# Kernel optimization log

Measured on AMD Instinct MI355X. Metric: run time of the kernel, lower is better.

## Reference

```python
import jax, jax.numpy as jnp
import numpy as np

SHAPES = ((100, 100), (50, 50), (25, 25))  # (H, W) per level
B, D, NH, HD, NL, NP, DFF = 4, 256, 8, 32, 3, 4, 1024
L = sum(h * w for h, w in SHAPES)  # 13125
EPS = 1e-5


def _layer_norm(x, g, b):
    m = jnp.mean(x, axis=-1, keepdims=True)
    v = jnp.var(x, axis=-1, keepdims=True)
    return (x - m) * jax.lax.rsqrt(v + EPS) * g + b


def _grid_sample_bilinear(img, grid):
    """img: [N,C,H,W]; grid: [N,Lq,P,2] in [-1,1]; align_corners=False, zero pad.
    Returns [N,C,Lq,P]."""
    N, C, H, W = img.shape
    x = ((grid[..., 0] + 1.0) * W - 1.0) * 0.5
    y = ((grid[..., 1] + 1.0) * H - 1.0) * 0.5
    x0 = jnp.floor(x); y0 = jnp.floor(y)
    x1 = x0 + 1.0; y1 = y0 + 1.0
    wx1 = x - x0; wx0 = 1.0 - wx1
    wy1 = y - y0; wy0 = 1.0 - wy1
    flat = img.reshape(N, C, H * W)

    def gather(ix, iy):
        valid = ((ix >= 0) & (ix < W) & (iy >= 0) & (iy < H)).astype(img.dtype)
        ii = (jnp.clip(iy, 0, H - 1).astype(jnp.int32) * W
              + jnp.clip(ix, 0, W - 1).astype(jnp.int32))  # [N,Lq,P]
        idx = jnp.broadcast_to(ii.reshape(N, 1, -1), (N, C, ii.shape[1] * ii.shape[2]))
        vals = jnp.take_along_axis(flat, idx, axis=2).reshape(N, C, ii.shape[1], ii.shape[2])
        return vals * valid[:, None]

    out = (gather(x0, y0) * (wx0 * wy0)[:, None]
           + gather(x1, y0) * (wx1 * wy0)[:, None]
           + gather(x0, y1) * (wx0 * wy1)[:, None]
           + gather(x1, y1) * (wx1 * wy1)[:, None])
    return out


def _ms_deform_attn_core(value, loc, attn):
    """value: [B,L,NH,HD]; loc: [B,Lq,NH,NL,NP,2] in [0,1]; attn: [B,Lq,NH,NL,NP]."""
    Bn, Lq = loc.shape[0], loc.shape[1]
    grids = 2.0 * loc - 1.0
    start = 0
    samples = []
    for lid, (H, W) in enumerate(SHAPES):
        v = value[:, start:start + H * W]            # [B,HW,NH,HD]
        start += H * W
        v = v.transpose(0, 2, 3, 1).reshape(Bn * NH, HD, H, W)
        g = grids[:, :, :, lid].transpose(0, 2, 1, 3, 4).reshape(Bn * NH, Lq, NP, 2)
        samples.append(_grid_sample_bilinear(v, g))  # [B*NH,HD,Lq,NP]
    sv = jnp.stack(samples, axis=-2).reshape(Bn * NH, HD, Lq, NL * NP)
    a = attn.transpose(0, 2, 1, 3, 4).reshape(Bn * NH, 1, Lq, NL * NP)
    out = (sv * a).sum(-1)                            # [B*NH,HD,Lq]
    return out.reshape(Bn, NH * HD, Lq).transpose(0, 2, 1)


def setup_inputs() -> dict:
    key = jax.random.key(0)
    ks = jax.random.split(key, 16)
    f32 = jnp.float32
    inp = {
        'src': jax.random.normal(ks[0], (B, L, D), f32),
        'pos': jax.random.normal(ks[1], (B, L, D), f32),
        'reference_points': jax.random.uniform(ks[2], (B, L, NL, 2), f32),
        'Wv': jax.random.normal(ks[3], (D, D), f32) * 0.02,
        'bv': jnp.zeros((D,), f32),
        'Woff': jax.random.normal(ks[4], (D, NH * NL * NP * 2), f32) * 0.02,
        'boff': jax.random.normal(ks[5], (NH * NL * NP * 2,), f32) * 0.5,
        'Wattn': jax.random.normal(ks[6], (D, NH * NL * NP), f32) * 0.02,
        'battn': jnp.zeros((NH * NL * NP,), f32),
        'Wout': jax.random.normal(ks[7], (D, D), f32) * 0.02,
        'bout': jnp.zeros((D,), f32),
        'g1': jnp.ones((D,), f32), 'b1': jnp.zeros((D,), f32),
        'Wff1': jax.random.normal(ks[8], (D, DFF), f32) * 0.02,
        'bff1': jnp.zeros((DFF,), f32),
        'Wff2': jax.random.normal(ks[9], (DFF, D), f32) * 0.02,
        'bff2': jnp.zeros((D,), f32),
        'g2': jnp.ones((D,), f32), 'b2': jnp.zeros((D,), f32),
    }
    return inp


def reference(src, pos, reference_points, Wv, bv, Woff, boff, Wattn, battn,
              Wout, bout, g1, b1, Wff1, bff1, Wff2, bff2, g2, b2):
    # DeformableTransformerEncoderLayer forward (eval mode: dropout = identity)
    q = src + pos
    value = (src @ Wv + bv).reshape(B, L, NH, HD)
    off = (q @ Woff + boff).reshape(B, L, NH, NL, NP, 2)
    attn = jax.nn.softmax((q @ Wattn + battn).reshape(B, L, NH, NL * NP), axis=-1)
    attn = attn.reshape(B, L, NH, NL, NP)
    norm = jnp.array([[w, h] for h, w in SHAPES], dtype=src.dtype)  # [NL,2] = (W,H)
    loc = reference_points[:, :, None, :, None, :] + off / norm[None, None, None, :, None, :]
    attn_out = _ms_deform_attn_core(value, loc, attn) @ Wout + bout
    x = _layer_norm(src + attn_out, g1, b1)
    ff = jax.nn.relu(x @ Wff1 + bff1) @ Wff2 + bff2
    return _layer_norm(x + ff, g2, b2)
```

## Files before the change

### kernel.cpp

```cpp
#include <hip/hip_runtime.h>


#define BLTOK 52500
#define MP    52608
#define LSP   13125

using short8  = __attribute__((ext_vector_type(8))) short;
using ushort8v= __attribute__((ext_vector_type(8))) unsigned short;
using f32x4   = __attribute__((ext_vector_type(4))) float;
using fl2     = __attribute__((ext_vector_type(2))) float;

__device__ __forceinline__ ushort f2b(float f) {
  union { float f; unsigned u; } x; x.f = f;
  unsigned r = (x.u + 0x7fffu + ((x.u >> 16) & 1u)) >> 16;
  return (ushort)r;
}
__device__ __forceinline__ float b2f(ushort h) {
  union { unsigned u; float f; } x; x.u = ((unsigned)h) << 16;
  return x.f;
}

#define GLDS16(gp, lp) __builtin_amdgcn_global_load_lds( \
    (const __attribute__((address_space(1))) void*)(gp), \
    (__attribute__((address_space(3))) void*)(lp), 16, 0, 0)

__global__ __launch_bounds__(256) void prep_weights(
    const float* __restrict__ Wv, const float* __restrict__ Woff,
    const float* __restrict__ Wattn, const float* __restrict__ Wout,
    const float* __restrict__ Wff1, const float* __restrict__ Wff2,
    const float* __restrict__ boff, const float* __restrict__ battn,
    ushort* __restrict__ wv_t, ushort* __restrict__ wcat_t,
    ushort* __restrict__ wout_t, ushort* __restrict__ wff1_t,
    ushort* __restrict__ wff2_t, float* __restrict__ bcat)
{
  int i = blockIdx.x * 256 + threadIdx.x;
  if (i < 65536) {
    int n = i >> 8, k = i & 255;
    wv_t[i] = f2b(Wv[k * 256 + n]);
    return;
  }
  int j = i - 65536;
  if (j < 98304) {
    int n = j >> 8, k = j & 255;
    float v = (n < 192) ? Woff[k * 192 + n]
            : (n < 288) ? Wattn[k * 96 + (n - 192)] : 0.f;
    wcat_t[j] = f2b(v);
    return;
  }
  j -= 98304;
  if (j < 65536) {
    int n = j >> 8, k = j & 255;
    wout_t[j] = f2b(Wout[k * 256 + n]);
    return;
  }
  j -= 65536;
  if (j < 262144) {
    int n = j >> 8, k = j & 255;
    wff1_t[j] = f2b(Wff1[k * 1024 + n]);
    return;
  }
  j -= 262144;
  if (j < 262144) {
    int n = j >> 10, k = j & 1023;
    wff2_t[j] = f2b(Wff2[k * 256 + n]);
    return;
  }
  j -= 262144;
  if (j < 384) bcat[j] = (j < 192) ? boff[j] : (j < 288) ? battn[j - 192] : 0.f;
}

__global__ __launch_bounds__(256) void prep_act(
    const float* __restrict__ src, const float* __restrict__ pos,
    ushort* __restrict__ src_bf, ushort* __restrict__ q_bf)
{
  const size_t e = ((size_t)blockIdx.x * 256 + threadIdx.x) * 4;
  if (e >= (size_t)MP * 256) return;
  ushort4 sb, qb;
  if (e < (size_t)BLTOK * 256) {
    const float4 s = *(const float4*)(src + e);
    const float4 p = *(const float4*)(pos + e);
    sb.x = f2b(s.x); sb.y = f2b(s.y); sb.z = f2b(s.z); sb.w = f2b(s.w);
    qb.x = f2b(s.x + p.x); qb.y = f2b(s.y + p.y);
    qb.z = f2b(s.z + p.z); qb.w = f2b(s.w + p.w);
  } else {
    sb.x = sb.y = sb.z = sb.w = 0;
    qb.x = qb.y = qb.z = qb.w = 0;
  }
  *(ushort4*)(src_bf + e) = sb;
  *(ushort4*)(q_bf + e) = qb;
}

template <int EPI>
__global__ __launch_bounds__(256) void gemm128(
    const ushort* __restrict__ A, const ushort* __restrict__ Bt,
    const float* __restrict__ bias, const float* __restrict__ addf,
    const ushort* __restrict__ addb, ushort* __restrict__ C,
    int Mact, int Nact, int Nstr, int K)
{
  __shared__ __align__(16) ushort sm[16384];
  ushort* As = sm;
  ushort* Bs = sm + 8192;
  float*  epf = (float*)sm;
  const int tid = threadIdx.x;
  const int wave = tid >> 6, lane = tid & 63;
  const int n0 = blockIdx.x * 128, m0 = blockIdx.y * 128;
  const int srow = lane >> 2, skc = (lane & 3) * 8;
  const ushort* Ag = A + (size_t)(m0 + wave * 32 + srow) * K + skc;
  const ushort* Bg = Bt + (size_t)(n0 + wave * 32 + srow) * K + skc;
  const int quad = lane >> 4, l16 = lane & 15;
  const int wm = (wave & 1) * 64, wn = (wave >> 1) * 64;
  f32x4 acc[4][4] = {};

#define STAGE(buf, kk) { \
    ushort* la = As + (buf) * 4096 + wave * 1024; \
    ushort* lb = Bs + (buf) * 4096 + wave * 1024; \
    GLDS16(Ag + (kk), la); \
    GLDS16(Ag + (kk) + 16 * K, la + 512); \
    GLDS16(Bg + (kk), lb); \
    GLDS16(Bg + (kk) + 16 * K, lb + 512); }

  STAGE(0, 0);
  int cur = 0;
  for (int k0 = 0; k0 < K; k0 += 32) {
    __syncthreads();
    if (k0 + 32 < K) STAGE(cur ^ 1, k0 + 32);
    const ushort* Ab = As + cur * 4096;
    const ushort* Bb = Bs + cur * 4096;
    short8 af[4], bf[4];
#pragma unroll
    for (int i = 0; i < 4; i++)
      af[i] = *(const short8*)(&Ab[(wm + i * 16 + l16) * 32 + quad * 8]);
#pragma unroll
    for (int j = 0; j < 4; j++)
      bf[j] = *(const short8*)(&Bb[(wn + j * 16 + l16) * 32 + quad * 8]);
#pragma unroll
    for (int i = 0; i < 4; i++)
#pragma unroll
      for (int j = 0; j < 4; j++)
        acc[i][j] = __builtin_amdgcn_mfma_f32_16x16x32_bf16(af[i], bf[j],
                                                            acc[i][j], 0, 0, 0);
    cur ^= 1;
  }
#undef STAGE

  for (int half = 0; half < 2; half++) {
    __syncthreads();
    if ((wave & 1) == half) {
#pragma unroll
      for (int i = 0; i < 4; i++)
#pragma unroll
        for (int j = 0; j < 4; j++)
#pragma unroll
          for (int r = 0; r < 4; r++)
            epf[(i * 16 + quad * 4 + r) * 128 + wn + j * 16 + l16] = acc[i][j][r];
    }
    __syncthreads();
    const int gm0 = m0 + half * 64;
#pragma unroll
    for (int g = 0; g < 4; g++) {
      const int lrow = g * 16 + (tid >> 4);
      const int col0 = (tid & 15) * 8;
      const int grow = gm0 + lrow;
      const int gcol = n0 + col0;
      if (grow < Mact && gcol < Nact) {
        float v[8];
#pragma unroll
        for (int c = 0; c < 8; c++) v[c] = epf[lrow * 128 + col0 + c] + bias[gcol + c];
        const size_t idx = (size_t)grow * Nstr + gcol;
        if (EPI == 1) {
          const float4 a0 = *(const float4*)(addf + idx);
          const float4 a1 = *(const float4*)(addf + idx + 4);
          v[0] += a0.x; v[1] += a0.y; v[2] += a0.z; v[3] += a0.w;
          v[4] += a1.x; v[5] += a1.y; v[6] += a1.z; v[7] += a1.w;
        }
        if (EPI == 2) {
#pragma unroll
          for (int c = 0; c < 8; c++) v[c] = fmaxf(v[c], 0.f);
        }
        if (EPI == 3) {
          const ushort8v ab = *(const ushort8v*)(addb + idx);
#pragma unroll
          for (int c = 0; c < 8; c++) v[c] += b2f(ab[c]);
        }
        ushort8v o;
#pragma unroll
        for (int c = 0; c < 8; c++) o[c] = f2b(v[c]);
        *(ushort8v*)(C + idx) = o;
      }
    }
  }
}

__global__ __launch_bounds__(256) void deform_sample(
    const ushort* __restrict__ value, const ushort* __restrict__ oa_all,
    const float* __restrict__ refp, ushort* __restrict__ outb)
{
  const int tid = threadIdx.x;
  const int tok = blockIdx.x * 8 + (tid >> 5);
  if (tok >= BLTOK) return;
  const int b = tok / LSP;
  const int l = tid & 31;
  const int h = l >> 2;
  const ushort* oa = oa_all + (uint)tok * 320u;
  const float* rp = refp + (uint)tok * 6u;
  const uint base = (uint)b * (LSP * 256u) + (uint)(l * 8);
  const int Wl[3] = {100, 50, 25};
  const int Stl[3] = {0, 10000, 12500};

  const ushort* lg = oa + 192 + h * 12;
  float w[12], mx = -1e30f;
#pragma unroll
  for (int i = 0; i < 12; i++) { w[i] = b2f(lg[i]); mx = fmaxf(mx, w[i]); }
  float s = 0.f;
#pragma unroll
  for (int i = 0; i < 12; i++) { w[i] = expf(w[i] - mx); s += w[i]; }
  const float inv = 1.f / s;

  fl2 acc2[4] = {};
#pragma unroll
  for (int lid = 0; lid < 3; lid++) {
    const int W = Wl[lid], st = Stl[lid];
    const float Wf = (float)W;
    const float rx = rp[lid * 2], ry = rp[lid * 2 + 1];
#pragma unroll
    for (int p = 0; p < 4; p++) {
      const uint oxy = *(const uint*)(oa + h * 24 + lid * 8 + p * 2);
      union { uint u; float f; } ux, uy;
      ux.u = oxy << 16;
      uy.u = oxy & 0xffff0000u;
      const float aw = w[lid * 4 + p] * inv;
      const float x = (rx + ux.f / Wf) * Wf - 0.5f;
      const float y = (ry + uy.f / Wf) * Wf - 0.5f;
      const float x0f = floorf(x), y0f = floorf(y);
      const float wx1 = x - x0f, wy1 = y - y0f;
      const float wx0 = 1.f - wx1, wy0 = 1.f - wy1;
      const int ix0 = (int)x0f, iy0 = (int)y0f;
      const bool x0v = (ix0 >= 0) & (ix0 < W);
      const bool x1v = (ix0 + 1 >= 0) & (ix0 + 1 < W);
      const bool y0v = (iy0 >= 0) & (iy0 < W);
      const bool y1v = (iy0 + 1 >= 0) & (iy0 + 1 < W);
      const float ay0 = aw * wy0, ay1 = aw * wy1;
      const float w00 = (x0v & y0v) ? ay0 * wx0 : 0.f;
      const float w10 = (x1v & y0v) ? ay0 * wx1 : 0.f;
      const float w01 = (x0v & y1v) ? ay1 * wx0 : 0.f;
      const float w11 = (x1v & y1v) ? ay1 * wx1 : 0.f;
      const int ix0c = min(max(ix0, 0), W - 1);
      const int ix1c = min(max(ix0 + 1, 0), W - 1);
      const int iy0c = min(max(iy0, 0), W - 1);
      const int iy1c = min(max(iy0 + 1, 0), W - 1);
      const uint r00 = (uint)(st + iy0c * W + ix0c) * 256u;
      const uint r10 = (uint)(st + iy0c * W + ix1c) * 256u;
      const uint r01 = (uint)(st + iy1c * W + ix0c) * 256u;
      const uint r11 = (uint)(st + iy1c * W + ix1c) * 256u;
      const uint4 q00 = *(const uint4*)(value + base + r00);
      const uint4 q10 = *(const uint4*)(value + base + r10);
      const uint4 q01 = *(const uint4*)(value + base + r01);
      const uint4 q11 = *(const uint4*)(value + base + r11);
      const fl2 w00v = {w00, w00}, w10v = {w10, w10};
      const fl2 w01v = {w01, w01}, w11v = {w11, w11};
      const uint* u00 = (const uint*)&q00;
      const uint* u10 = (const uint*)&q10;
      const uint* u01 = (const uint*)&q01;
      const uint* u11 = (const uint*)&q11;
#pragma unroll
      for (int pp = 0; pp < 4; pp++) {
        union { uint u; float f; } a, bb2, cc, dd, a2, b2u, c2, d2;
        a.u  = u00[pp] << 16;  a2.u  = u00[pp] & 0xffff0000u;
        bb2.u= u10[pp] << 16;  b2u.u = u10[pp] & 0xffff0000u;
        cc.u = u01[pp] << 16;  c2.u  = u01[pp] & 0xffff0000u;
        dd.u = u11[pp] << 16;  d2.u  = u11[pp] & 0xffff0000u;
        fl2 v00 = {a.f, a2.f}, v10 = {bb2.f, b2u.f};
        fl2 v01 = {cc.f, c2.f}, v11 = {dd.f, d2.f};
        acc2[pp] += w00v * v00 + w10v * v10 + w01v * v01 + w11v * v11;
      }
    }
  }
  ushort4 o0, o1;
  o0.x = f2b(acc2[0].x); o0.y = f2b(acc2[0].y);
  o0.z = f2b(acc2[1].x); o0.w = f2b(acc2[1].y);
  o1.x = f2b(acc2[2].x); o1.y = f2b(acc2[2].y);
  o1.z = f2b(acc2[3].x); o1.w = f2b(acc2[3].y);
  ushort* op = outb + (uint)tok * 256u + (uint)(l * 8);
  *(ushort4*)op = o0;
  *(ushort4*)(op + 4) = o1;
}

template <int OUTF>
__global__ __launch_bounds__(256) void ln256(
    const ushort* __restrict__ in, const float* __restrict__ gg,
    const float* __restrict__ bb, ushort* __restrict__ outb,
    float* __restrict__ outf, int rows)
{
  const int wave = threadIdx.x >> 6, lane = threadIdx.x & 63;
  const int r = blockIdx.x * 4 + wave;
  if (r >= rows) return;
  const ushort* rowp = in + (size_t)r * 256;
  const ushort4 u = *(const ushort4*)(rowp + lane * 4);
  float v[4] = {b2f(u.x), b2f(u.y), b2f(u.z), b2f(u.w)};
  float s = v[0] + v[1] + v[2] + v[3];
  float s2 = v[0] * v[0] + v[1] * v[1] + v[2] * v[2] + v[3] * v[3];
#pragma unroll
  for (int o = 32; o > 0; o >>= 1) {
    s += __shfl_xor(s, o);
    s2 += __shfl_xor(s2, o);
  }
  const float mean = s * (1.f / 256.f);
  const float var = s2 * (1.f / 256.f) - mean * mean;
  const float rstd = rsqrtf(var + 1e-5f);
#pragma unroll
  for (int j = 0; j < 4; j++) {
    const int col = lane * 4 + j;
    const float o = (v[j] - mean) * rstd * gg[col] + bb[col];
    if (OUTF) outf[(size_t)r * 256 + col] = o;
    else outb[(size_t)r * 256 + col] = f2b(o);
  }
}

extern "C" void kernel_launch(void* const* d_in, const int* in_sizes, int n_in,
                              void* d_out, int out_size, void* d_ws, size_t ws_size,
                              hipStream_t stream)
{
  const float* src   = (const float*)d_in[0];
  const float* pos   = (const float*)d_in[1];
  const float* refp  = (const float*)d_in[2];
  const float* Wv    = (const float*)d_in[3];
  const float* bv    = (const float*)d_in[4];
  const float* Woff  = (const float*)d_in[5];
  const float* boff  = (const float*)d_in[6];
  const float* Wattn = (const float*)d_in[7];
  const float* battn = (const float*)d_in[8];
  const float* Wout  = (const float*)d_in[9];
  const float* bout  = (const float*)d_in[10];
  const float* g1    = (const float*)d_in[11];
  const float* b1    = (const float*)d_in[12];
  const float* Wff1  = (const float*)d_in[13];
  const float* bff1  = (const float*)d_in[14];
  const float* Wff2  = (const float*)d_in[15];
  const float* bff2  = (const float*)d_in[16];
  const float* g2    = (const float*)d_in[17];
  const float* b2    = (const float*)d_in[18];
  float* out = (float*)d_out;
  char* ws = (char*)d_ws;

  ushort* wcat_t = (ushort*)(ws + 0);
  ushort* wff1_t = (ushort*)(ws + 196608);
  ushort* wff2_t = (ushort*)(ws + 720896);
  float*  bcat   = (float*)(ws + 1245184);
  ushort* A1 = (ushort*)(ws + 1246720);
  ushort* A2 = (ushort*)(ws + 28182016);
  ushort* A3 = (ushort*)(ws + 55117312);
  ushort* A4 = (ushort*)(ws + 81997312);
  ushort* A5 = (ushort*)(ws + 115597312);
  ushort* wout_t = (ushort*)(ws + 223076352);
  ushort* wv_t   = (ushort*)(ws + 223207424);

  prep_weights<<<2946, 256, 0, stream>>>(Wv, Woff, Wattn, Wout, Wff1, Wff2,
                                         boff, battn,
                                         wv_t, wcat_t, wout_t, wff1_t, wff2_t, bcat);
  prep_act<<<MP / 4, 256, 0, stream>>>(src, pos, A1, A2);
  gemm128<0><<<dim3(2, MP / 128), 256, 0, stream>>>(A1, wv_t, bv, nullptr, nullptr,
                                                    A3, BLTOK, 256, 256, 256);
  gemm128<0><<<dim3(3, MP / 128), 256, 0, stream>>>(A2, wcat_t, bcat, nullptr, nullptr,
                                                    A4, BLTOK, 320, 320, 256);
  deform_sample<<<(BLTOK + 7) / 8, 256, 0, stream>>>(A3, A4, refp, A5);
  gemm128<3><<<dim3(2, MP / 128), 256, 0, stream>>>(A5, wout_t, bout, nullptr, A1,
                                                    A4, BLTOK, 256, 256, 256);
  ln256<0><<<BLTOK / 4, 256, 0, stream>>>(A4, g1, b1, A2, nullptr, BLTOK);
  gemm128<2><<<dim3(8, MP / 128), 256, 0, stream>>>(A2, wff1_t, bff1, nullptr, nullptr,
                                                    A5, MP, 1024, 1024, 256);
  gemm128<3><<<dim3(2, MP / 128), 256, 0, stream>>>(A5, wff2_t, bff2, nullptr, A2,
                                                    A3, BLTOK, 256, 256, 1024);
  ln256<1><<<BLTOK / 4, 256, 0, stream>>>(A3, g2, b2, nullptr, out, BLTOK);
}
```

Before: 478.5 us.

## Map one thread per head in deform sampling with vectorized offset loads

The deformable sampling kernel now gives each thread a whole head (32 channels) for one token, so one block covers 32 tokens instead of 8. Each thread computes the offsets and softmax for its head once, rather than four threads repeating that work. Offsets and logits come in with wide vector loads, and the location maths drops a divide and multiply because the normalisation cancels. The cost is four times as many gather loads and accumulators per thread, which raises register pressure and cuts memory-level parallelism across threads. It also uses fast exp and a hardware reciprocal.

```diff
diff --git a/kernel.cpp b/kernel.cpp
--- a/kernel.cpp
+++ b/kernel.cpp
@@ -17,6 +17,14 @@
 }
 __device__ __forceinline__ float b2f(ushort h) {
   union { unsigned u; float f; } x; x.u = ((unsigned)h) << 16;
+  return x.f;
+}
+__device__ __forceinline__ float blo(uint u) {
+  union { unsigned u; float f; } x; x.u = u << 16;
+  return x.f;
+}
+__device__ __forceinline__ float bhi(uint u) {
+  union { unsigned u; float f; } x; x.u = u & 0xffff0000u;
   return x.f;
 }
 
@@ -196,41 +204,51 @@
     const float* __restrict__ refp, ushort* __restrict__ outb)
 {
   const int tid = threadIdx.x;
-  const int tok = blockIdx.x * 8 + (tid >> 5);
+  const int tok = blockIdx.x * 32 + (tid >> 3);
   if (tok >= BLTOK) return;
   const int b = tok / LSP;
-  const int l = tid & 31;
-  const int h = l >> 2;
+  const int h = tid & 7;
   const ushort* oa = oa_all + (uint)tok * 320u;
   const float* rp = refp + (uint)tok * 6u;
-  const uint base = (uint)b * (LSP * 256u) + (uint)(l * 8);
+  const uint base = (uint)b * (LSP * 256u) + (uint)(h * 32);
+
+  const uint4 oq0 = *(const uint4*)(oa + h * 24);
+  const uint4 oq1 = *(const uint4*)(oa + h * 24 + 8);
+  const uint4 oq2 = *(const uint4*)(oa + h * 24 + 16);
+  const uint oxy[12] = {oq0.x, oq0.y, oq0.z, oq0.w,
+                        oq1.x, oq1.y, oq1.z, oq1.w,
+                        oq2.x, oq2.y, oq2.z, oq2.w};
+
+  const ushort* lgp = oa + 192 + h * 12;
+  const uint2 lq0 = *(const uint2*)(lgp);
+  const uint2 lq1 = *(const uint2*)(lgp + 4);
+  const uint2 lq2 = *(const uint2*)(lgp + 8);
+  float w[12] = {blo(lq0.x), bhi(lq0.x), blo(lq0.y), bhi(lq0.y),
+                 blo(lq1.x), bhi(lq1.x), blo(lq1.y), bhi(lq1.y),
+                 blo(lq2.x), bhi(lq2.x), blo(lq2.y), bhi(lq2.y)};
+  float mx = -1e30f;
+#pragma unroll
+  for (int i = 0; i < 12; i++) mx = fmaxf(mx, w[i]);
+  float s = 0.f;
+#pragma unroll
+  for (int i = 0; i < 12; i++) { w[i] = __expf(w[i] - mx); s += w[i]; }
+  const float inv = __builtin_amdgcn_rcpf(s);
+
   const int Wl[3] = {100, 50, 25};
   const int Stl[3] = {0, 10000, 12500};
-
-  const ushort* lg = oa + 192 + h * 12;
-  float w[12], mx = -1e30f;
-#pragma unroll
-  for (int i = 0; i < 12; i++) { w[i] = b2f(lg[i]); mx = fmaxf(mx, w[i]); }
-  float s = 0.f;
-#pragma unroll
-  for (int i = 0; i < 12; i++) { w[i] = expf(w[i] - mx); s += w[i]; }
-  const float inv = 1.f / s;
-
-  fl2 acc2[4] = {};
+  fl2 acc[16] = {};
 #pragma unroll
   for (int lid = 0; lid < 3; lid++) {
     const int W = Wl[lid], st = Stl[lid];
     const float Wf = (float)W;
-    const float rx = rp[lid * 2], ry = rp[lid * 2 + 1];
+    const float rxw = rp[lid * 2] * Wf - 0.5f;
+    const float ryw = rp[lid * 2 + 1] * Wf - 0.5f;
 #pragma unroll
     for (int p = 0; p < 4; p++) {
-      const uint oxy = *(const uint*)(oa + h * 24 + lid * 8 + p * 2);
-      union { uint u; float f; } ux, uy;
-      ux.u = oxy << 16;
-      uy.u = oxy & 0xffff0000u;
+      const uint o = oxy[lid * 4 + p];
       const float aw = w[lid * 4 + p] * inv;
-      const float x = (rx + ux.f / Wf) * Wf - 0.5f;
-      const float y = (ry + uy.f / Wf) * Wf - 0.5f;
+      const float x = rxw + blo(o);
+      const float y = ryw + bhi(o);
       const float x0f = floorf(x), y0f = floorf(y);
       const float wx1 = x - x0f, wy1 = y - y0f;
       const float wx0 = 1.f - wx1, wy0 = 1.f - wy1;
@@ -248,41 +266,44 @@
       const int ix1c = min(max(ix0 + 1, 0), W - 1);
       const int iy0c = min(max(iy0, 0), W - 1);
       const int iy1c = min(max(iy0 + 1, 0), W - 1);
-      const uint r00 = (uint)(st + iy0c * W + ix0c) * 256u;
-      const uint r10 = (uint)(st + iy0c * W + ix1c) * 256u;
-      const uint r01 = (uint)(st + iy1c * W + ix0c) * 256u;
-      const uint r11 = (uint)(st + iy1c * W + ix1c) * 256u;
-      const uint4 q00 = *(const uint4*)(value + base + r00);
-      const uint4 q10 = *(const uint4*)(value + base + r10);
-      const uint4 q01 = *(const uint4*)(value + base + r01);
-      const uint4 q11 = *(const uint4*)(value + base + r11);
+      const ushort* p00 = value + base + (uint)(st + iy0c * W + ix0c) * 256u;
+      const ushort* p10 = value + base + (uint)(st + iy0c * W + ix1c) * 256u;
+      const ushort* p01 = value + base + (uint)(st + iy1c * W + ix0c) * 256u;
+      const ushort* p11 = value + base + (uint)(st + iy1c * W + ix1c) * 256u;
       const fl2 w00v = {w00, w00}, w10v = {w10, w10};
       const fl2 w01v = {w01, w01}, w11v = {w11, w11};
-      const uint* u00 = (const uint*)&q00;
-      const uint* u10 = (const uint*)&q10;
-      const uint* u01 = (const uint*)&q01;
-      const uint* u11 = (const uint*)&q11;
-#pragma unroll
-      for (int pp = 0; pp < 4; pp++) {
-        union { uint u; float f; } a, bb2, cc, dd, a2, b2u, c2, d2;
-        a.u  = u00[pp] << 16;  a2.u  = u00[pp] & 0xffff0000u;
-        bb2.u= u10[pp] << 16;  b2u.u = u10[pp] & 0xffff0000u;
-        cc.u = u01[pp] << 16;  c2.u  = u01[pp] & 0xffff0000u;
-        dd.u = u11[pp] << 16;  d2.u  = u11[pp] & 0xffff0000u;
-        fl2 v00 = {a.f, a2.f}, v10 = {bb2.f, b2u.f};
-        fl2 v01 = {cc.f, c2.f}, v11 = {dd.f, d2.f};
-        acc2[pp] += w00v * v00 + w10v * v10 + w01v * v01 + w11v * v11;
+#pragma unroll
+      for (int j = 0; j < 4; j++) {
+        const uint4 q00 = *(const uint4*)(p00 + j * 8);
+        const uint4 q10 = *(const uint4*)(p10 + j * 8);
+        const uint4 q01 = *(const uint4*)(p01 + j * 8);
+        const uint4 q11 = *(const uint4*)(p11 + j * 8);
+        const uint* u00 = (const uint*)&q00;
+        const uint* u10 = (const uint*)&q10;
+        const uint* u01 = (const uint*)&q01;
+        const uint* u11 = (const uint*)&q11;
+#pragma unroll
+        for (int e = 0; e < 4; e++) {
+          const fl2 v00 = {blo(u00[e]), bhi(u00[e])};
+          const fl2 v10 = {blo(u10[e]), bhi(u10[e])};
+          const fl2 v01 = {blo(u01[e]), bhi(u01[e])};
+          const fl2 v11 = {blo(u11[e]), bhi(u11[e])};
+          acc[j * 4 + e] += w00v * v00 + w10v * v10 + w01v * v01 + w11v * v11;
+        }
       }
     }
   }
-  ushort4 o0, o1;
-  o0.x = f2b(acc2[0].x); o0.y = f2b(acc2[0].y);
-  o0.z = f2b(acc2[1].x); o0.w = f2b(acc2[1].y);
-  o1.x = f2b(acc2[2].x); o1.y = f2b(acc2[2].y);
-  o1.z = f2b(acc2[3].x); o1.w = f2b(acc2[3].y);
-  ushort* op = outb + (uint)tok * 256u + (uint)(l * 8);
-  *(ushort4*)op = o0;
-  *(ushort4*)(op + 4) = o1;
+  ushort* op = outb + (uint)tok * 256u + (uint)(h * 32);
+#pragma unroll
+  for (int j = 0; j < 4; j++) {
+    ushort8v o;
+#pragma unroll
+    for (int e = 0; e < 4; e++) {
+      o[e * 2]     = f2b(acc[j * 4 + e].x);
+      o[e * 2 + 1] = f2b(acc[j * 4 + e].y);
+    }
+    *(ushort8v*)(op + j * 8) = o;
+  }
 }
 
 template <int OUTF>
@@ -362,7 +383,7 @@
                                                     A3, BLTOK, 256, 256, 256);
   gemm128<0><<<dim3(3, MP / 128), 256, 0, stream>>>(A2, wcat_t, bcat, nullptr, nullptr,
                                                     A4, BLTOK, 320, 320, 256);
-  deform_sample<<<(BLTOK + 7) / 8, 256, 0, stream>>>(A3, A4, refp, A5);
+  deform_sample<<<(BLTOK + 31) / 32, 256, 0, stream>>>(A3, A4, refp, A5);
   gemm128<3><<<dim3(2, MP / 128), 256, 0, stream>>>(A5, wout_t, bout, nullptr, A1,
                                                     A4, BLTOK, 256, 256, 256);
   ln256<0><<<BLTOK / 4, 256, 0, stream>>>(A4, g1, b1, A2, nullptr, BLTOK);
```

After: 645.9 us. 1.35x slower.

## Map deform-sample blocks per XCD by batch and pipeline bilinear gathers

Applied to the files above, without the earlier changes.

Block indices are remapped so each of the 8 XCDs processes half of one batch, keeping that batch's value tensor resident in its L2. The sampling-point coordinate and weight math is split across the 4 lanes sharing a head, with the softmax done via quad shuffles and results broadcast by shuffle instead of recomputed redundantly. Gathers are double-buffered, so the loads for the next point are issued before the current point is accumulated. This adds shuffle traffic and register pressure, and assumes a round-robin block-to-XCD dispatch.

```diff
diff --git a/kernel.cpp b/kernel.cpp
--- a/kernel.cpp
+++ b/kernel.cpp
@@ -17,6 +17,14 @@
 }
 __device__ __forceinline__ float b2f(ushort h) {
   union { unsigned u; float f; } x; x.u = ((unsigned)h) << 16;
+  return x.f;
+}
+__device__ __forceinline__ float blo(uint u) {
+  union { unsigned u; float f; } x; x.u = u << 16;
+  return x.f;
+}
+__device__ __forceinline__ float bhi(uint u) {
+  union { unsigned u; float f; } x; x.u = u & 0xffff0000u;
   return x.f;
 }
 
@@ -196,85 +204,107 @@
     const float* __restrict__ refp, ushort* __restrict__ outb)
 {
   const int tid = threadIdx.x;
-  const int tok = blockIdx.x * 8 + (tid >> 5);
-  if (tok >= BLTOK) return;
-  const int b = tok / LSP;
+  const int xcd  = blockIdx.x & 7;
+  const int slot = blockIdx.x >> 3;
+  const int batch = xcd >> 1, halfb = xcd & 1;
+  const int tok = batch * LSP + halfb * 6564 + slot * 8 + (tid >> 5);
+  const int tokEnd = batch * LSP + (halfb ? LSP : 6564);
+  if (tok >= tokEnd) return;
   const int l = tid & 31;
   const int h = l >> 2;
+  const int q = l & 3;
   const ushort* oa = oa_all + (uint)tok * 320u;
   const float* rp = refp + (uint)tok * 6u;
-  const uint base = (uint)b * (LSP * 256u) + (uint)(l * 8);
+  const uint base = (uint)batch * (LSP * 256u) + (uint)(l * 8);
+
   const int Wl[3] = {100, 50, 25};
   const int Stl[3] = {0, 10000, 12500};
 
-  const ushort* lg = oa + 192 + h * 12;
-  float w[12], mx = -1e30f;
-#pragma unroll
-  for (int i = 0; i < 12; i++) { w[i] = b2f(lg[i]); mx = fmaxf(mx, w[i]); }
-  float s = 0.f;
-#pragma unroll
-  for (int i = 0; i < 12; i++) { w[i] = expf(w[i] - mx); s += w[i]; }
-  const float inv = 1.f / s;
-
-  fl2 acc2[4] = {};
+  const ushort* lgp = oa + 192 + h * 12 + q;
+  float e0 = b2f(lgp[0]), e1 = b2f(lgp[4]), e2 = b2f(lgp[8]);
+  float m3 = fmaxf(fmaxf(e0, e1), e2);
+  m3 = fmaxf(m3, __shfl_xor(m3, 1, 4));
+  m3 = fmaxf(m3, __shfl_xor(m3, 2, 4));
+  e0 = __expf(e0 - m3); e1 = __expf(e1 - m3); e2 = __expf(e2 - m3);
+  float s3 = e0 + e1 + e2;
+  s3 += __shfl_xor(s3, 1, 4);
+  s3 += __shfl_xor(s3, 2, 4);
+  const float inv = __builtin_amdgcn_rcpf(s3);
+  const float awn[3] = {e0 * inv, e1 * inv, e2 * inv};
+
+  float ow[3][4];
+  uint  orr[3][4];
 #pragma unroll
   for (int lid = 0; lid < 3; lid++) {
     const int W = Wl[lid], st = Stl[lid];
     const float Wf = (float)W;
-    const float rx = rp[lid * 2], ry = rp[lid * 2 + 1];
-#pragma unroll
-    for (int p = 0; p < 4; p++) {
-      const uint oxy = *(const uint*)(oa + h * 24 + lid * 8 + p * 2);
-      union { uint u; float f; } ux, uy;
-      ux.u = oxy << 16;
-      uy.u = oxy & 0xffff0000u;
-      const float aw = w[lid * 4 + p] * inv;
-      const float x = (rx + ux.f / Wf) * Wf - 0.5f;
-      const float y = (ry + uy.f / Wf) * Wf - 0.5f;
-      const float x0f = floorf(x), y0f = floorf(y);
-      const float wx1 = x - x0f, wy1 = y - y0f;
-      const float wx0 = 1.f - wx1, wy0 = 1.f - wy1;
-      const int ix0 = (int)x0f, iy0 = (int)y0f;
-      const bool x0v = (ix0 >= 0) & (ix0 < W);
-      const bool x1v = (ix0 + 1 >= 0) & (ix0 + 1 < W);
-      const bool y0v = (iy0 >= 0) & (iy0 < W);
-      const bool y1v = (iy0 + 1 >= 0) & (iy0 + 1 < W);
-      const float ay0 = aw * wy0, ay1 = aw * wy1;
-      const float w00 = (x0v & y0v) ? ay0 * wx0 : 0.f;
-      const float w10 = (x1v & y0v) ? ay0 * wx1 : 0.f;
-      const float w01 = (x0v & y1v) ? ay1 * wx0 : 0.f;
-      const float w11 = (x1v & y1v) ? ay1 * wx1 : 0.f;
-      const int ix0c = min(max(ix0, 0), W - 1);
-      const int ix1c = min(max(ix0 + 1, 0), W - 1);
-      const int iy0c = min(max(iy0, 0), W - 1);
-      const int iy1c = min(max(iy0 + 1, 0), W - 1);
-      const uint r00 = (uint)(st + iy0c * W + ix0c) * 256u;
-      const uint r10 = (uint)(st + iy0c * W + ix1c) * 256u;
-      const uint r01 = (uint)(st + iy1c * W + ix0c) * 256u;
-      const uint r11 = (uint)(st + iy1c * W + ix1c) * 256u;
-      const uint4 q00 = *(const uint4*)(value + base + r00);
-      const uint4 q10 = *(const uint4*)(value + base + r10);
-      const uint4 q01 = *(const uint4*)(value + base + r01);
-      const uint4 q11 = *(const uint4*)(value + base + r11);
-      const fl2 w00v = {w00, w00}, w10v = {w10, w10};
-      const fl2 w01v = {w01, w01}, w11v = {w11, w11};
-      const uint* u00 = (const uint*)&q00;
-      const uint* u10 = (const uint*)&q10;
-      const uint* u01 = (const uint*)&q01;
-      const uint* u11 = (const uint*)&q11;
-#pragma unroll
-      for (int pp = 0; pp < 4; pp++) {
-        union { uint u; float f; } a, bb2, cc, dd, a2, b2u, c2, d2;
-        a.u  = u00[pp] << 16;  a2.u  = u00[pp] & 0xffff0000u;
-        bb2.u= u10[pp] << 16;  b2u.u = u10[pp] & 0xffff0000u;
-        cc.u = u01[pp] << 16;  c2.u  = u01[pp] & 0xffff0000u;
-        dd.u = u11[pp] << 16;  d2.u  = u11[pp] & 0xffff0000u;
-        fl2 v00 = {a.f, a2.f}, v10 = {bb2.f, b2u.f};
-        fl2 v01 = {cc.f, c2.f}, v11 = {dd.f, d2.f};
-        acc2[pp] += w00v * v00 + w10v * v10 + w01v * v01 + w11v * v11;
-      }
-    }
-  }
+    const uint o = *(const uint*)(oa + h * 24 + lid * 8 + q * 2);
+    const float aw = awn[lid];
+    const float x = rp[lid * 2] * Wf - 0.5f + blo(o);
+    const float y = rp[lid * 2 + 1] * Wf - 0.5f + bhi(o);
+    const float x0f = floorf(x), y0f = floorf(y);
+    const float wx1 = x - x0f, wy1 = y - y0f;
+    const float wx0 = 1.f - wx1, wy0 = 1.f - wy1;
+    const int ix0 = (int)x0f, iy0 = (int)y0f;
+    const bool x0v = (ix0 >= 0) & (ix0 < W);
+    const bool x1v = (ix0 + 1 >= 0) & (ix0 + 1 < W);
+    const bool y0v = (iy0 >= 0) & (iy0 < W);
+    const bool y1v = (iy0 + 1 >= 0) & (iy0 + 1 < W);
+    const float ay0 = aw * wy0, ay1 = aw * wy1;
+    ow[lid][0] = (x0v & y0v) ? ay0 * wx0 : 0.f;
+    ow[lid][1] = (x1v & y0v) ? ay0 * wx1 : 0.f;
+    ow[lid][2] = (x0v & y1v) ? ay1 * wx0 : 0.f;
+    ow[lid][3] = (x1v & y1v) ? ay1 * wx1 : 0.f;
+    const int ix0c = min(max(ix0, 0), W - 1);
+    const int ix1c = min(max(ix0 + 1, 0), W - 1);
+    const int iy0c = min(max(iy0, 0), W - 1);
+    const int iy1c = min(max(iy0 + 1, 0), W - 1);
+    orr[lid][0] = (uint)(st + iy0c * W + ix0c) * 256u;
+    orr[lid][1] = (uint)(st + iy0c * W + ix1c) * 256u;
+    orr[lid][2] = (uint)(st + iy1c * W + ix0c) * 256u;
+    orr[lid][3] = (uint)(st + iy1c * W + ix1c) * 256u;
+  }
+
+  fl2 acc2[4] = {};
+  float bww[2][4];
+  uint4 cq[2][4];
+
+#define PRE(p, s) { \
+    const int lid_ = (p) >> 2, own_ = (p) & 3; \
+    bww[s][0] = __shfl(ow[lid_][0], own_, 4); \
+    bww[s][1] = __shfl(ow[lid_][1], own_, 4); \
+    bww[s][2] = __shfl(ow[lid_][2], own_, 4); \
+    bww[s][3] = __shfl(ow[lid_][3], own_, 4); \
+    const uint r0_ = (uint)__shfl((int)orr[lid_][0], own_, 4); \
+    const uint r1_ = (uint)__shfl((int)orr[lid_][1], own_, 4); \
+    const uint r2_ = (uint)__shfl((int)orr[lid_][2], own_, 4); \
+    const uint r3_ = (uint)__shfl((int)orr[lid_][3], own_, 4); \
+    cq[s][0] = *(const uint4*)(value + base + r0_); \
+    cq[s][1] = *(const uint4*)(value + base + r1_); \
+    cq[s][2] = *(const uint4*)(value + base + r2_); \
+    cq[s][3] = *(const uint4*)(value + base + r3_); }
+
+#define CONS(s) { \
+    _Pragma("unroll") \
+    for (int c_ = 0; c_ < 4; c_++) { \
+      const fl2 wv_ = {bww[s][c_], bww[s][c_]}; \
+      const uint* u_ = (const uint*)&cq[s][c_]; \
+      _Pragma("unroll") \
+      for (int pp_ = 0; pp_ < 4; pp_++) { \
+        const fl2 vv_ = {blo(u_[pp_]), bhi(u_[pp_])}; \
+        acc2[pp_] += wv_ * vv_; \
+      } \
+    } }
+
+  PRE(0, 0);
+#pragma unroll
+  for (int p = 0; p < 12; p++) {
+    if (p < 11) PRE(p + 1, (p + 1) & 1);
+    CONS(p & 1);
+  }
+#undef PRE
+#undef CONS
+
   ushort4 o0, o1;
   o0.x = f2b(acc2[0].x); o0.y = f2b(acc2[0].y);
   o0.z = f2b(acc2[1].x); o0.w = f2b(acc2[1].y);
@@ -362,7 +392,7 @@
                                                     A3, BLTOK, 256, 256, 256);
   gemm128<0><<<dim3(3, MP / 128), 256, 0, stream>>>(A2, wcat_t, bcat, nullptr, nullptr,
                                                     A4, BLTOK, 320, 320, 256);
-  deform_sample<<<(BLTOK + 7) / 8, 256, 0, stream>>>(A3, A4, refp, A5);
+  deform_sample<<<8 * 821, 256, 0, stream>>>(A3, A4, refp, A5);
   gemm128<3><<<dim3(2, MP / 128), 256, 0, stream>>>(A5, wout_t, bout, nullptr, A1,
                                                     A4, BLTOK, 256, 256, 256);
   ln256<0><<<BLTOK / 4, 256, 0, stream>>>(A4, g1, b1, A2, nullptr, BLTOK);
```

Result: no change. 475.2 us (-0.7%).
